# Kernel optimization log

Measured on AMD Instinct MI355X. Metric: run time of the kernel, lower is better.

Reference implementation:

```python
import jax, jax.numpy as jnp
import numpy as np

NEG = -1000000.0  # mask fill value used by the torch module


def setup_inputs() -> dict:
    key = jax.random.key(0)
    kq, kk, kv, km = jax.random.split(key, 4)
    B, Q, K, D = 8, 2048, 2048, 128
    queries = jax.random.normal(kq, (B, Q, D), dtype=jnp.float32)
    keys = jax.random.normal(kk, (B, K, D), dtype=jnp.float32)
    values = jax.random.normal(kv, (B, K, D), dtype=jnp.float32)
    attntion_mask = jax.random.randint(km, (B, K), 0, 2, dtype=jnp.int32)
    return {"queries": queries, "keys": keys, "values": values,
            "attntion_mask": attntion_mask}


def reference(queries, keys, values, attntion_mask):
    d = queries.shape[-1]
    # scores: [B, Q, K]
    scores = jnp.einsum('bqd,bkd->bqk', queries, keys) / jnp.sqrt(
        jnp.asarray(d, dtype=queries.dtype))
    # 2D mask [B, K] broadcasts over the query axis (torch repeat_interleave)
    mask = attntion_mask.astype(bool)[:, None, :]  # [B, 1, K]
    scores = jnp.where(mask, scores, NEG)
    weights = jax.nn.softmax(scores, axis=-1)
    # dropout rate is 0.0 (eval mode) -> identity
    return jnp.einsum('bqk,bkv->bqv', weights, values)
```

## Files before the change

### kernel.cpp

```cpp
#include <hip/hip_runtime.h>
#include <stdint.h>

typedef __attribute__((ext_vector_type(8))) short short8;
typedef __attribute__((ext_vector_type(4))) float f32x4;

#define NB 8
#define NQ 2048
#define NK 2048
#define ND 128
#define SCALE 0.08838834764831845f
#define L2E   1.4426950408889634f
#define FMAXC 10.0f

__device__ __forceinline__ uint32_t pk_bf16(float a, float b) {
  uint32_t ua = __builtin_bit_cast(uint32_t, a);
  uint32_t ub = __builtin_bit_cast(uint32_t, b);
  ua += 0x7FFFu + ((ua >> 16) & 1u);
  ub += 0x7FFFu + ((ub >> 16) & 1u);
  return (ua >> 16) | (ub & 0xFFFF0000u);
}

__device__ __forceinline__ void dma16(const void* g, void* l) {
  __builtin_amdgcn_global_load_lds((const __attribute__((address_space(1))) void*)g,
                                   (__attribute__((address_space(3))) void*)l, 16, 0, 0);
}

__global__ __launch_bounds__(256) void compact_kernel(const int* __restrict__ maskm,
                                                      int* __restrict__ idxArr,
                                                      int* __restrict__ KcArr) {
  __shared__ int cnt;
  const int b = blockIdx.x;
  const int t = threadIdx.x;
  const int lane = t & 63;
  if (t == 0) cnt = 0;
  __syncthreads();
#pragma unroll
  for (int j = 0; j < 8; ++j) {
    int k = t * 8 + j;
    bool bit = maskm[b * NK + k] != 0;
    unsigned long long m = __ballot(bit);
    int pre = __popcll(m & ((1ull << lane) - 1ull));
    int tot = __popcll(m);
    int base = 0;
    if (lane == 0 && tot) base = atomicAdd(&cnt, tot);
    base = __shfl(base, 0);
    if (bit) idxArr[b * NK + base + pre] = k;
  }
  __syncthreads();
  int kc = cnt;
  for (int s = kc + t; s < NK; s += 256) idxArr[b * NK + s] = -1;
  if (t == 0) KcArr[b] = kc;
}

__global__ __launch_bounds__(256) void prep_kernel(const float* __restrict__ v,
                                                   const float* __restrict__ kin,
                                                   ushort* __restrict__ vt,
                                                   ushort* __restrict__ kb,
                                                   const int* __restrict__ idxArr) {
  const int t = threadIdx.x;
  const int bid = blockIdx.x;
  if (bid < 512) {
    __shared__ __align__(16) float tile[4096];
    char* sm = (char*)tile;
    const int b = bid >> 6;
    const int k0 = ((bid >> 1) & 31) << 6;
    const int d0 = (bid & 1) << 6;
#pragma unroll
    for (int i = 0; i < 4; ++i) {
      int id = i * 256 + t;
      int k = id >> 4, c = id & 15;
      int src = idxArr[b * NK + k0 + k];
      uint4 val; val.x = 0u; val.y = 0u; val.z = 0u; val.w = 0u;
      if (src >= 0) val = *(const uint4*)(v + (size_t)(b * NK + src) * ND + d0 + c * 4);
      *(uint4*)(sm + k * 256 + ((c ^ (k & 15)) * 16)) = val;
    }
    __syncthreads();
#pragma unroll
    for (int i = 0; i < 2; ++i) {
      int id = i * 256 + t;
      int d = id >> 3, kc = id & 7;
      uint32_t w[4];
#pragma unroll
      for (int jj = 0; jj < 4; ++jj) {
        int kA = kc * 8 + jj * 2, kB = kA + 1;
        float fa = *(const float*)(sm + kA * 256 + (((d >> 2) ^ (kA & 15)) * 16) + (d & 3) * 4);
        float fb = *(const float*)(sm + kB * 256 + (((d >> 2) ^ (kB & 15)) * 16) + (d & 3) * 4);
        w[jj] = pk_bf16(fa, fb);
      }
      uint4 o; o.x = w[0]; o.y = w[1]; o.z = w[2]; o.w = w[3];
      *(uint4*)(vt + (size_t)(b * ND + d0 + d) * NK + k0 + kc * 8) = o;
    }
  } else {
    int gs = (bid - 512) * 16 + (t >> 4);
    int src = idxArr[gs];
    int col = (t & 15) * 8;
    uint4 u; u.x = 0u; u.y = 0u; u.z = 0u; u.w = 0u;
    if (src >= 0) {
      int b2 = gs >> 11;
      const float* p = kin + (size_t)(b2 * NK + src) * ND + col;
      f32x4 a = *(const f32x4*)p;
      f32x4 c = *(const f32x4*)(p + 4);
      u.x = pk_bf16(a[0], a[1]); u.y = pk_bf16(a[2], a[3]);
      u.z = pk_bf16(c[0], c[1]); u.w = pk_bf16(c[2], c[3]);
    }
    *(uint4*)(kb + (size_t)gs * ND + col) = u;
  }
}

template <bool MASKED>
__device__ __forceinline__ void do_softmax(const f32x4 st[2], float& l_,
                                           char* pbase, int r, int quad, int rem) {
  const float C1 = SCALE * L2E;
  const float C2 = -FMAXC * L2E;
  float p[2][4]; float ps = 0.f;
#pragma unroll
  for (int mt = 0; mt < 2; ++mt) {
    float t0 = fmaf(st[mt][0], C1, C2);
    float t1 = fmaf(st[mt][1], C1, C2);
    float t2 = fmaf(st[mt][2], C1, C2);
    float t3 = fmaf(st[mt][3], C1, C2);
    if (MASKED) {
      const int rm = rem - mt * 16;
      t0 = (rm > 0) ? t0 : -2.0e6f;
      t1 = (rm > 1) ? t1 : -2.0e6f;
      t2 = (rm > 2) ? t2 : -2.0e6f;
      t3 = (rm > 3) ? t3 : -2.0e6f;
    }
    p[mt][0] = exp2f(t0); p[mt][1] = exp2f(t1);
    p[mt][2] = exp2f(t2); p[mt][3] = exp2f(t3);
    ps += p[mt][0] + p[mt][1] + p[mt][2] + p[mt][3];
  }
  l_ += ps;
#pragma unroll
  for (int mt = 0; mt < 2; ++mt) {
    uint2 w; w.x = pk_bf16(p[mt][0], p[mt][1]); w.y = pk_bf16(p[mt][2], p[mt][3]);
    *(uint2*)(pbase + r * 64 + (((mt * 4 + quad) ^ (r & 6)) * 8)) = w;
  }
}

#define LDS_BYTES 139264
__global__ __launch_bounds__(512) void attn_kernel(const float* __restrict__ qm,
                                                   const ushort* __restrict__ kbm,
                                                   const ushort* __restrict__ vtm,
                                                   const int* __restrict__ KcArr,
                                                   float* __restrict__ outm) {
  __shared__ __align__(16) char sm[LDS_BYTES];
  const int o   = blockIdx.x;
  const int bid = (o & 7) * 32 + (o >> 3);
  const int b   = bid >> 5;
  const int q0  = (bid & 31) << 6;
  const int t = threadIdx.x;
  const int lane = t & 63;
  const int wave = t >> 6;
  const int r = lane & 15;
  const int quad = lane >> 4;
  const int qg = wave >> 2;
  const int kq = wave & 3;

  const int Kc   = KcArr[b];
  const int n_it = (Kc + 127) >> 7;

  uint32_t koff[4], voff[4];
#pragma unroll
  for (int j = 0; j < 4; ++j) {
    int i = wave * 4 + j;
    int rho = i * 4 + (lane >> 4);
    int ck = (lane & 15) ^ (rho & 15);
    koff[j] = (uint32_t)(b * NK + rho) * ND + ck * 8;
    int u = i * 16 + (lane >> 2);
    int cv = (lane & 3) ^ (u & 3);
    voff[j] = (uint32_t)(b * ND + (u & 127)) * NK + (u >> 7) * 32 + cv * 8;
  }

#define ISSUE_K(tt, bufi)                                                       \
  {                                                                             \
    const uint32_t kadd_ = (uint32_t)(tt) * 128 * ND;                           \
    char* kb_ = sm + (bufi) * 32768;                                            \
    _Pragma("unroll")                                                           \
    for (int j = 0; j < 4; ++j)                                                 \
      dma16(kbm + koff[j] + kadd_, kb_ + (wave * 4 + j) * 1024);                \
  }
#define ISSUE_V(tt)                                                             \
  {                                                                             \
    const uint32_t vadd_ = (uint32_t)(tt) * 128;                                \
    _Pragma("unroll")                                                           \
    for (int j = 0; j < 4; ++j)                                                 \
      dma16(vtm + voff[j] + vadd_, sm + 98304 + (wave * 4 + j) * 1024);         \
  }

  f32x4 qraw[2][4][2];
#pragma unroll
  for (int qt = 0; qt < 2; ++qt)
#pragma unroll
    for (int ks = 0; ks < 4; ++ks) {
      const float* p = qm + (size_t)(b * NQ + q0 + qg * 32 + qt * 16 + r) * ND + ks * 32 + quad * 8;
      qraw[qt][ks][0] = *(const f32x4*)p;
      qraw[qt][ks][1] = *(const f32x4*)(p + 4);
    }
  ISSUE_K(0, 0);
  if (n_it > 1) ISSUE_K(1, 1);
  short8 qf[2][4];
#pragma unroll
  for (int qt = 0; qt < 2; ++qt)
#pragma unroll
    for (int ks = 0; ks < 4; ++ks) {
      uint4 u;
      u.x = pk_bf16(qraw[qt][ks][0][0], qraw[qt][ks][0][1]);
      u.y = pk_bf16(qraw[qt][ks][0][2], qraw[qt][ks][0][3]);
      u.z = pk_bf16(qraw[qt][ks][1][0], qraw[qt][ks][1][1]);
      u.w = pk_bf16(qraw[qt][ks][1][2], qraw[qt][ks][1][3]);
      qf[qt][ks] = __builtin_bit_cast(short8, u);
    }

  f32x4 oacc[2][8];
#pragma unroll
  for (int qt = 0; qt < 2; ++qt)
#pragma unroll
    for (int dt = 0; dt < 8; ++dt) oacc[qt][dt] = (f32x4){0.f, 0.f, 0.f, 0.f};
  float l_[2] = {0.f, 0.f};

  char* const pbase = sm + 131072 + wave * 1024;
  char* const vbuf  = sm + 98304 + kq * 8192;

  int cur = 0;
  for (int it = 0; it < n_it; ++it) {
    if (it + 1 < n_it) asm volatile("s_waitcnt vmcnt(4)" ::: "memory");
    else               asm volatile("s_waitcnt vmcnt(0)" ::: "memory");
    __builtin_amdgcn_sched_barrier(0);
    __builtin_amdgcn_s_barrier();
    __builtin_amdgcn_sched_barrier(0);

    ISSUE_V(it);
    if (it + 2 < n_it) {
      int b2 = cur + 2; if (b2 >= 3) b2 -= 3;
      ISSUE_K(it + 2, b2);
    }

    char* const kcur = sm + cur * 32768 + kq * 8192;

    f32x4 st[2][2];
#pragma unroll
    for (int mt = 0; mt < 2; ++mt) {
      short8 kf[4];
#pragma unroll
      for (int ks = 0; ks < 4; ++ks)
        kf[ks] = *(const short8*)(kcur + (mt * 16 + r) * 256 + (((ks * 4 + quad) ^ r) * 16));
#pragma unroll
      for (int qt = 0; qt < 2; ++qt) {
        f32x4 acc = (f32x4){0.f, 0.f, 0.f, 0.f};
#pragma unroll
        for (int ks = 0; ks < 4; ++ks)
          acc = __builtin_amdgcn_mfma_f32_16x16x32_bf16(kf[ks], qf[qt][ks], acc, 0, 0, 0);
        st[mt][qt] = acc;
      }
    }

    const int vlim = Kc - it * 128 - kq * 32;
    short8 pf[2];
#pragma unroll
    for (int qt = 0; qt < 2; ++qt) {
      f32x4 s2[2] = { st[0][qt], st[1][qt] };
      if (vlim >= 32) do_softmax<false>(s2, l_[qt], pbase, r, quad, 0);
      else            do_softmax<true >(s2, l_[qt], pbase, r, quad, vlim - quad * 4);
      pf[qt] = *(const short8*)(pbase + r * 64 + (((quad * 2) ^ (r & 6)) * 8));
    }

    if (it + 2 < n_it) asm volatile("s_waitcnt vmcnt(4)" ::: "memory");
    else               asm volatile("s_waitcnt vmcnt(0)" ::: "memory");
    __builtin_amdgcn_sched_barrier(0);
    __builtin_amdgcn_s_barrier();
    __builtin_amdgcn_sched_barrier(0);

#pragma unroll
    for (int dt = 0; dt < 8; ++dt) {
      short8 vf = *(const short8*)(vbuf + (dt * 16 + r) * 64 + ((quad ^ (r & 3)) * 16));
#pragma unroll
      for (int qt = 0; qt < 2; ++qt)
        oacc[qt][dt] = __builtin_amdgcn_mfma_f32_16x16x32_bf16(vf, pf[qt], oacc[qt][dt], 0, 0, 0);
    }

    cur = (cur == 2) ? 0 : cur + 1;
  }

  __syncthreads();
  if (kq != 0) {
    float* xch = (float*)(sm + (qg * 3 + (kq - 1)) * 17408) + lane * 68;
    xch[0] = l_[0]; xch[1] = l_[1];
#pragma unroll
    for (int qt = 0; qt < 2; ++qt)
#pragma unroll
      for (int dt = 0; dt < 8; ++dt)
        *(f32x4*)(xch + 4 + (qt * 8 + dt) * 4) = oacc[qt][dt];
  }
  __syncthreads();
  if (kq == 0) {
    float* x0 = (float*)(sm + (qg * 3 + 0) * 17408) + lane * 68;
    float* x1 = (float*)(sm + (qg * 3 + 1) * 17408) + lane * 68;
    float* x2 = (float*)(sm + (qg * 3 + 2) * 17408) + lane * 68;
#pragma unroll
    for (int qt = 0; qt < 2; ++qt) {
      const int qrow = b * NQ + q0 + qg * 32 + qt * 16 + r;
      float ls = l_[qt] + x0[qt] + x1[qt] + x2[qt];
      ls += __shfl_xor(ls, 16);
      ls += __shfl_xor(ls, 32);
      float inv = 1.0f / ls;
#pragma unroll
      for (int dt = 0; dt < 8; ++dt) {
        f32x4 o1 = *(const f32x4*)(x0 + 4 + (qt * 8 + dt) * 4);
        f32x4 o2 = *(const f32x4*)(x1 + 4 + (qt * 8 + dt) * 4);
        f32x4 o3 = *(const f32x4*)(x2 + 4 + (qt * 8 + dt) * 4);
        f32x4 ov = oacc[qt][dt];
        ov[0] = (ov[0] + o1[0] + o2[0] + o3[0]) * inv;
        ov[1] = (ov[1] + o1[1] + o2[1] + o3[1]) * inv;
        ov[2] = (ov[2] + o1[2] + o2[2] + o3[2]) * inv;
        ov[3] = (ov[3] + o1[3] + o2[3] + o3[3]) * inv;
        *(f32x4*)(outm + (size_t)qrow * ND + dt * 16 + quad * 4) = ov;
      }
    }
  }
#undef ISSUE_K
#undef ISSUE_V
}

extern "C" void kernel_launch(void* const* d_in, const int* in_sizes, int n_in,
                              void* d_out, int out_size, void* d_ws, size_t ws_size,
                              hipStream_t stream) {
  const float* q   = (const float*)d_in[0];
  const float* k   = (const float*)d_in[1];
  const float* v   = (const float*)d_in[2];
  const int*   msk = (const int*)d_in[3];
  float* out = (float*)d_out;
  ushort* kb = (ushort*)d_ws;
  ushort* vt = kb + (size_t)NB * NK * ND;
  int* idxA  = (int*)(vt + (size_t)NB * NK * ND);
  int* kcA   = idxA + (size_t)NB * NK;

  compact_kernel<<<NB, 256, 0, stream>>>(msk, idxA, kcA);
  prep_kernel<<<1536, 256, 0, stream>>>(v, k, vt, kb, idxA);
  attn_kernel<<<256, 512, 0, stream>>>(q, kb, vt, kcA, out);
}
```

Baseline: 105.0 us.

## Halve attention block to 32 queries and 4 waves with contiguous key halves

```diff
diff --git a/kernel.cpp b/kernel.cpp
--- a/kernel.cpp
+++ b/kernel.cpp
@@ -138,27 +138,28 @@
   }
 }
 
-#define LDS_BYTES 139264
-__global__ __launch_bounds__(512) void attn_kernel(const float* __restrict__ qm,
+#define LDS_BYTES 69632
+__global__ __launch_bounds__(256) void attn_kernel(const float* __restrict__ qm,
                                                    const ushort* __restrict__ kbm,
                                                    const ushort* __restrict__ vtm,
                                                    const int* __restrict__ KcArr,
                                                    float* __restrict__ outm) {
   __shared__ __align__(16) char sm[LDS_BYTES];
   const int o   = blockIdx.x;
-  const int bid = (o & 7) * 32 + (o >> 3);
-  const int b   = bid >> 5;
-  const int q0  = (bid & 31) << 6;
+  const int bid = (o & 7) * 64 + (o >> 3);
+  const int b   = bid >> 6;
+  const int q0  = (bid & 63) << 5;
   const int t = threadIdx.x;
   const int lane = t & 63;
   const int wave = t >> 6;
   const int r = lane & 15;
   const int quad = lane >> 4;
-  const int qg = wave >> 2;
-  const int kq = wave & 3;
+  const int qg = wave >> 1;
+  const int kq = wave & 1;
 
   const int Kc   = KcArr[b];
-  const int n_it = (Kc + 127) >> 7;
+  const int n_it = (Kc + 63) >> 6;
+  const int CH   = n_it << 5;
 
   uint32_t koff[4], voff[4];
 #pragma unroll
@@ -166,61 +167,57 @@
     int i = wave * 4 + j;
     int rho = i * 4 + (lane >> 4);
     int ck = (lane & 15) ^ (rho & 15);
-    koff[j] = (uint32_t)(b * NK + rho) * ND + ck * 8;
+    koff[j] = (uint32_t)(b * NK + (rho >> 5) * CH + (rho & 31)) * ND + ck * 8;
     int u = i * 16 + (lane >> 2);
     int cv = (lane & 3) ^ (u & 3);
-    voff[j] = (uint32_t)(b * ND + (u & 127)) * NK + (u >> 7) * 32 + cv * 8;
+    voff[j] = (uint32_t)(b * ND + (u & 127)) * NK + (u >> 7) * CH + cv * 8;
   }
 
 #define ISSUE_K(tt, bufi)                                                       \
   {                                                                             \
-    const uint32_t kadd_ = (uint32_t)(tt) * 128 * ND;                           \
-    char* kb_ = sm + (bufi) * 32768;                                            \
+    const uint32_t kadd_ = (uint32_t)(tt) * 32 * ND;                            \
+    char* kb_ = sm + (bufi) * 16384;                                            \
     _Pragma("unroll")                                                           \
     for (int j = 0; j < 4; ++j)                                                 \
       dma16(kbm + koff[j] + kadd_, kb_ + (wave * 4 + j) * 1024);                \
   }
 #define ISSUE_V(tt)                                                             \
   {                                                                             \
-    const uint32_t vadd_ = (uint32_t)(tt) * 128;                                \
+    const uint32_t vadd_ = (uint32_t)(tt) * 32;                                 \
     _Pragma("unroll")                                                           \
     for (int j = 0; j < 4; ++j)                                                 \
-      dma16(vtm + voff[j] + vadd_, sm + 98304 + (wave * 4 + j) * 1024);         \
-  }
-
-  f32x4 qraw[2][4][2];
-#pragma unroll
-  for (int qt = 0; qt < 2; ++qt)
-#pragma unroll
-    for (int ks = 0; ks < 4; ++ks) {
-      const float* p = qm + (size_t)(b * NQ + q0 + qg * 32 + qt * 16 + r) * ND + ks * 32 + quad * 8;
-      qraw[qt][ks][0] = *(const f32x4*)p;
-      qraw[qt][ks][1] = *(const f32x4*)(p + 4);
-    }
+      dma16(vtm + voff[j] + vadd_, sm + 49152 + (wave * 4 + j) * 1024);         \
+  }
+
+  f32x4 qraw[4][2];
+#pragma unroll
+  for (int ks = 0; ks < 4; ++ks) {
+    const float* p = qm + (size_t)(b * NQ + q0 + qg * 16 + r) * ND + ks * 32 + quad * 8;
+    qraw[ks][0] = *(const f32x4*)p;
+    qraw[ks][1] = *(const f32x4*)(p + 4);
+  }
   ISSUE_K(0, 0);
   if (n_it > 1) ISSUE_K(1, 1);
-  short8 qf[2][4];
-#pragma unroll
-  for (int qt = 0; qt < 2; ++qt)
-#pragma unroll
-    for (int ks = 0; ks < 4; ++ks) {
-      uint4 u;
-      u.x = pk_bf16(qraw[qt][ks][0][0], qraw[qt][ks][0][1]);
-      u.y = pk_bf16(qraw[qt][ks][0][2], qraw[qt][ks][0][3]);
-      u.z = pk_bf16(qraw[qt][ks][1][0], qraw[qt][ks][1][1]);
-      u.w = pk_bf16(qraw[qt][ks][1][2], qraw[qt][ks][1][3]);
-      qf[qt][ks] = __builtin_bit_cast(short8, u);
-    }
-
-  f32x4 oacc[2][8];
-#pragma unroll
-  for (int qt = 0; qt < 2; ++qt)
-#pragma unroll
-    for (int dt = 0; dt < 8; ++dt) oacc[qt][dt] = (f32x4){0.f, 0.f, 0.f, 0.f};
-  float l_[2] = {0.f, 0.f};
-
-  char* const pbase = sm + 131072 + wave * 1024;
-  char* const vbuf  = sm + 98304 + kq * 8192;
+  short8 qf[4];
+#pragma unroll
+  for (int ks = 0; ks < 4; ++ks) {
+    uint4 u;
+    u.x = pk_bf16(qraw[ks][0][0], qraw[ks][0][1]);
+    u.y = pk_bf16(qraw[ks][0][2], qraw[ks][0][3]);
+    u.z = pk_bf16(qraw[ks][1][0], qraw[ks][1][1]);
+    u.w = pk_bf16(qraw[ks][1][2], qraw[ks][1][3]);
+    qf[ks] = __builtin_bit_cast(short8, u);
+  }
+
+  f32x4 oacc[8];
+#pragma unroll
+  for (int dt = 0; dt < 8; ++dt) oacc[dt] = (f32x4){0.f, 0.f, 0.f, 0.f};
+  float l_ = 0.f;
+
+  char* const pbase = sm + 65536 + wave * 1024;
+  char* const vbuf  = sm + 49152 + kq * 8192;
+
+  const int vlim0 = Kc - kq * CH;
 
   int cur = 0;
   for (int it = 0; it < n_it; ++it) {
@@ -236,34 +233,26 @@
       ISSUE_K(it + 2, b2);
     }
 
-    char* const kcur = sm + cur * 32768 + kq * 8192;
-
-    f32x4 st[2][2];
+    char* const kcur = sm + cur * 16384 + kq * 8192;
+
+    f32x4 st[2];
 #pragma unroll
     for (int mt = 0; mt < 2; ++mt) {
       short8 kf[4];
 #pragma unroll
       for (int ks = 0; ks < 4; ++ks)
         kf[ks] = *(const short8*)(kcur + (mt * 16 + r) * 256 + (((ks * 4 + quad) ^ r) * 16));
-#pragma unroll
-      for (int qt = 0; qt < 2; ++qt) {
-        f32x4 acc = (f32x4){0.f, 0.f, 0.f, 0.f};
-#pragma unroll
-        for (int ks = 0; ks < 4; ++ks)
-          acc = __builtin_amdgcn_mfma_f32_16x16x32_bf16(kf[ks], qf[qt][ks], acc, 0, 0, 0);
-        st[mt][qt] = acc;
-      }
-    }
-
-    const int vlim = Kc - it * 128 - kq * 32;
-    short8 pf[2];
-#pragma unroll
-    for (int qt = 0; qt < 2; ++qt) {
-      f32x4 s2[2] = { st[0][qt], st[1][qt] };
-      if (vlim >= 32) do_softmax<false>(s2, l_[qt], pbase, r, quad, 0);
-      else            do_softmax<true >(s2, l_[qt], pbase, r, quad, vlim - quad * 4);
-      pf[qt] = *(const short8*)(pbase + r * 64 + (((quad * 2) ^ (r & 6)) * 8));
-    }
+      f32x4 acc = (f32x4){0.f, 0.f, 0.f, 0.f};
+#pragma unroll
+      for (int ks = 0; ks < 4; ++ks)
+        acc = __builtin_amdgcn_mfma_f32_16x16x32_bf16(kf[ks], qf[ks], acc, 0, 0, 0);
+      st[mt] = acc;
+    }
+
+    const int vlim = vlim0 - it * 32;
+    if (vlim >= 32) do_softmax<false>(st, l_, pbase, r, quad, 0);
+    else            do_softmax<true >(st, l_, pbase, r, quad, vlim - quad * 4);
+    short8 pf = *(const short8*)(pbase + r * 64 + (((quad * 2) ^ (r & 6)) * 8));
 
     if (it + 2 < n_it) asm volatile("s_waitcnt vmcnt(4)" ::: "memory");
     else               asm volatile("s_waitcnt vmcnt(0)" ::: "memory");
@@ -274,48 +263,36 @@
 #pragma unroll
     for (int dt = 0; dt < 8; ++dt) {
       short8 vf = *(const short8*)(vbuf + (dt * 16 + r) * 64 + ((quad ^ (r & 3)) * 16));
-#pragma unroll
-      for (int qt = 0; qt < 2; ++qt)
-        oacc[qt][dt] = __builtin_amdgcn_mfma_f32_16x16x32_bf16(vf, pf[qt], oacc[qt][dt], 0, 0, 0);
+      oacc[dt] = __builtin_amdgcn_mfma_f32_16x16x32_bf16(vf, pf, oacc[dt], 0, 0, 0);
     }
 
     cur = (cur == 2) ? 0 : cur + 1;
   }
 
   __syncthreads();
-  if (kq != 0) {
-    float* xch = (float*)(sm + (qg * 3 + (kq - 1)) * 17408) + lane * 68;
-    xch[0] = l_[0]; xch[1] = l_[1];
-#pragma unroll
-    for (int qt = 0; qt < 2; ++qt)
-#pragma unroll
-      for (int dt = 0; dt < 8; ++dt)
-        *(f32x4*)(xch + 4 + (qt * 8 + dt) * 4) = oacc[qt][dt];
+  float* xch = (float*)(sm + qg * 9216) + lane * 36;
+  if (kq == 1) {
+    xch[0] = l_;
+#pragma unroll
+    for (int dt = 0; dt < 8; ++dt)
+      *(f32x4*)(xch + 4 + dt * 4) = oacc[dt];
   }
   __syncthreads();
   if (kq == 0) {
-    float* x0 = (float*)(sm + (qg * 3 + 0) * 17408) + lane * 68;
-    float* x1 = (float*)(sm + (qg * 3 + 1) * 17408) + lane * 68;
-    float* x2 = (float*)(sm + (qg * 3 + 2) * 17408) + lane * 68;
-#pragma unroll
-    for (int qt = 0; qt < 2; ++qt) {
-      const int qrow = b * NQ + q0 + qg * 32 + qt * 16 + r;
-      float ls = l_[qt] + x0[qt] + x1[qt] + x2[qt];
-      ls += __shfl_xor(ls, 16);
-      ls += __shfl_xor(ls, 32);
-      float inv = 1.0f / ls;
-#pragma unroll
-      for (int dt = 0; dt < 8; ++dt) {
-        f32x4 o1 = *(const f32x4*)(x0 + 4 + (qt * 8 + dt) * 4);
-        f32x4 o2 = *(const f32x4*)(x1 + 4 + (qt * 8 + dt) * 4);
-        f32x4 o3 = *(const f32x4*)(x2 + 4 + (qt * 8 + dt) * 4);
-        f32x4 ov = oacc[qt][dt];
-        ov[0] = (ov[0] + o1[0] + o2[0] + o3[0]) * inv;
-        ov[1] = (ov[1] + o1[1] + o2[1] + o3[1]) * inv;
-        ov[2] = (ov[2] + o1[2] + o2[2] + o3[2]) * inv;
-        ov[3] = (ov[3] + o1[3] + o2[3] + o3[3]) * inv;
-        *(f32x4*)(outm + (size_t)qrow * ND + dt * 16 + quad * 4) = ov;
-      }
+    const int qrow = b * NQ + q0 + qg * 16 + r;
+    float ls = l_ + xch[0];
+    ls += __shfl_xor(ls, 16);
+    ls += __shfl_xor(ls, 32);
+    float inv = 1.0f / ls;
+#pragma unroll
+    for (int dt = 0; dt < 8; ++dt) {
+      f32x4 o1 = *(const f32x4*)(xch + 4 + dt * 4);
+      f32x4 ov = oacc[dt];
+      ov[0] = (ov[0] + o1[0]) * inv;
+      ov[1] = (ov[1] + o1[1]) * inv;
+      ov[2] = (ov[2] + o1[2]) * inv;
+      ov[3] = (ov[3] + o1[3]) * inv;
+      *(f32x4*)(outm + (size_t)qrow * ND + dt * 16 + quad * 4) = ov;
     }
   }
 #undef ISSUE_K
@@ -337,5 +314,5 @@
 
   compact_kernel<<<NB, 256, 0, stream>>>(msk, idxA, kcA);
   prep_kernel<<<1536, 256, 0, stream>>>(v, k, vt, kb, idxA);
-  attn_kernel<<<256, 512, 0, stream>>>(q, kb, vt, kcA, out);
-}
+  attn_kernel<<<512, 256, 0, stream>>>(q, kb, vt, kcA, out);
+}
```

New measurement: 105.0 us. Within noise of the previous version (+0.0%).
